# Kernel optimization log

Measured on AMD Instinct MI355X. Metric: run time of the kernel, lower is better.

## Reference

```python
import jax, jax.numpy as jnp
import numpy as np

B, N, D, TOP_K = 4, 4096, 256, 64
EPS = 1e-12  # F.normalize default eps


def setup_inputs() -> dict:
    key = jax.random.key(0)
    kx, kw, kb = jax.random.split(key, 3)
    x = jax.random.normal(kx, (B, N, D), dtype=jnp.float32)
    # value_fc: nn.Linear(in_dims, in_dims) -> weight [D, D], bias [D]
    lim = 1.0 / np.sqrt(D)
    W = jax.random.uniform(kw, (D, D), dtype=jnp.float32, minval=-lim, maxval=lim)
    b = jax.random.uniform(kb, (D,), dtype=jnp.float32, minval=-lim, maxval=lim)
    return {"x": x, "W": W, "b": b}


def reference(x, W, b):
    # value = value_fc(x)
    value = jnp.einsum("bnd,ed->bne", x, W) + b  # torch Linear: x @ W.T + b
    # F.normalize(x, p=2, dim=-1)
    norm = jnp.linalg.norm(x, axis=-1, keepdims=True)
    normed_x = x / jnp.maximum(norm, EPS)
    # full cosine-similarity matrix [B, N, N]
    cos_sim = jnp.einsum("bnd,bmd->bnm", normed_x, normed_x)
    # topk along last dim, scatter back into zeros
    topk_vals, topk_inds = jax.lax.top_k(cos_sim, TOP_K)  # [B, N, K]
    b_idx = jnp.arange(x.shape[0])[:, None, None]
    n_idx = jnp.arange(x.shape[1])[None, :, None]
    attn_sparse = jnp.zeros_like(cos_sim).at[b_idx, n_idx, topk_inds].set(topk_vals)
    # softmax over full row (zeros at non-topk positions contribute exp(0))
    attn = jax.nn.softmax(attn_sparse, axis=-1)
    return jnp.einsum("bnm,bmd->bnd", attn, value)
```

## Files before the change

### kernel.cpp

```cpp
#include <hip/hip_runtime.h>
#include <hip/hip_bf16.h>
#include <stdint.h>

#define B_ 4
#define N_ 4096
#define D_ 256
#define K_ 64
#define BN_ (B_*N_)

typedef __attribute__((ext_vector_type(8))) short bf16x8;
typedef __attribute__((ext_vector_type(8))) unsigned short u16x8;
typedef __attribute__((ext_vector_type(4))) float f32x4;
typedef __attribute__((address_space(1))) const unsigned int gas_u32;
typedef __attribute__((address_space(3))) unsigned int las_u32;

static __device__ __forceinline__ unsigned short f2bf(float f) {
  union { float f; unsigned u; } x; x.f = f;
  unsigned r = x.u + 0x7fffu + ((x.u >> 16) & 1u);
  return (unsigned short)(r >> 16);
}
static __device__ __forceinline__ float bf2f(unsigned short u) {
  union { unsigned u; float f; } x; x.u = ((unsigned)u) << 16;
  return x.f;
}
static __device__ __forceinline__ f32x4 mfma16(bf16x8 a, bf16x8 b, f32x4 c) {
  return __builtin_amdgcn_mfma_f32_16x16x32_bf16(a, b, c, 0, 0, 0);
}

__global__ __launch_bounds__(256) void prep_kernel(
    const float* __restrict__ x, const float* __restrict__ W,
    unsigned short* __restrict__ xn, float* __restrict__ norms,
    unsigned short* __restrict__ Wb, float* __restrict__ vsum) {
  const int bid = blockIdx.x;
  if (bid < 4096) {
    int row = bid * 4 + (threadIdx.x >> 6);
    int lane = threadIdx.x & 63;
    const float4 v = reinterpret_cast<const float4*>(x + (size_t)row * D_)[lane];
    float ss = v.x*v.x + v.y*v.y + v.z*v.z + v.w*v.w;
    #pragma unroll
    for (int off = 32; off > 0; off >>= 1) ss += __shfl_xor(ss, off);
    float nrm = sqrtf(ss);
    float scale = 1.0f / fmaxf(nrm, 1e-12f);
    ushort4 o;
    o.x = f2bf(v.x * scale); o.y = f2bf(v.y * scale);
    o.z = f2bf(v.z * scale); o.w = f2bf(v.w * scale);
    reinterpret_cast<ushort4*>(xn + (size_t)row * D_)[lane] = o;
    if (lane == 0) norms[row] = nrm;
  } else if (bid < 4160) {
    int i = (bid - 4096) * 256 + threadIdx.x;
    float4 v = reinterpret_cast<const float4*>(W)[i];
    ushort4 o; o.x = f2bf(v.x); o.y = f2bf(v.y); o.z = f2bf(v.z); o.w = f2bf(v.w);
    reinterpret_cast<ushort4*>(Wb)[i] = o;
  } else {
    reinterpret_cast<float4*>(vsum)[threadIdx.x] = (float4){0.f, 0.f, 0.f, 0.f};
  }
}

__global__ __launch_bounds__(256, 3) void compute_kernel(
    const unsigned short* __restrict__ xn, const float* __restrict__ norms,
    const unsigned short* __restrict__ Wb, const float* __restrict__ bias,
    unsigned short* __restrict__ value, float* __restrict__ vsum,
    unsigned short* __restrict__ S) {
  __shared__ __attribute__((aligned(16))) unsigned char smem[33792];
  unsigned char* As = smem;
  unsigned char* Bs = smem + 16384;
  float* ns_s   = (float*)(smem + 32768);
  float* bias_s = (float*)(smem + 33280);

  const int t = threadIdx.x, lane = t & 63, w = t >> 6;
  const int l15 = lane & 15, qv = lane >> 4, rb = qv * 4;
  const int wr = w >> 1, wc = w & 1;
  const int x7 = l15 & 7;

  const unsigned short* Asrc;
  const unsigned short* Bsrc;
  int rbG, cb, batch = 0;
  const bool vmode = (blockIdx.x < 256);
  if (vmode) {
    rbG = (blockIdx.x >> 1) * 128;
    cb  = (blockIdx.x & 1) * 128;
    Asrc = xn + (size_t)rbG * D_;
    Bsrc = Wb + (size_t)cb * D_;
    if (t < 128) { ns_s[t] = norms[rbG + t]; bias_s[t] = bias[cb + t]; }
  } else {
    int g = blockIdx.x - 256;
    batch = g >> 10;
    int tl = g & 1023;
    rbG = (tl >> 5) * 128;
    cb  = (tl & 31) * 128;
    Asrc = xn + ((size_t)batch * N_ + rbG) * D_;
    Bsrc = xn + ((size_t)batch * N_ + cb)  * D_;
  }

  f32x4 acc[4][4];
  #pragma unroll
  for (int i = 0; i < 4; i++)
    #pragma unroll
    for (int j = 0; j < 4; j++) acc[i][j] = (f32x4){0.f,0.f,0.f,0.f};

  for (int kk = 0; kk < 4; kk++) {
    #pragma unroll
    for (int p = 0; p < 4; p++) {
      int q = t + p * 256;
      int row = q >> 3, c = q & 7;
      int cg = (c ^ (row & 7)) * 8;
      __builtin_amdgcn_global_load_lds(
          (gas_u32*)(Asrc + (size_t)row * D_ + kk * 64 + cg),
          (las_u32*)(As + q * 16), 16, 0, 0);
      __builtin_amdgcn_global_load_lds(
          (gas_u32*)(Bsrc + (size_t)row * D_ + kk * 64 + cg),
          (las_u32*)(Bs + q * 16), 16, 0, 0);
    }
    __syncthreads();
    #pragma unroll
    for (int ks = 0; ks < 2; ks++) {
      const int cpos = (((ks * 4 + qv) ^ x7) << 4);
      bf16x8 a[4], bb[4];
      #pragma unroll
      for (int rt = 0; rt < 4; rt++)
        a[rt] = *(const bf16x8*)(As + (wr*64 + rt*16 + l15) * 128 + cpos);
      #pragma unroll
      for (int ct = 0; ct < 4; ct++)
        bb[ct] = *(const bf16x8*)(Bs + (wc*64 + ct*16 + l15) * 128 + cpos);
      #pragma unroll
      for (int rt = 0; rt < 4; rt++)
        #pragma unroll
        for (int ct = 0; ct < 4; ct++)
          acc[rt][ct] = mfma16(a[rt], bb[ct], acc[rt][ct]);
    }
    __syncthreads();
  }

  unsigned short* kbuf = (unsigned short*)smem;
  if (vmode) {
    float vpart[4] = {0.f, 0.f, 0.f, 0.f};
    #pragma unroll
    for (int rt = 0; rt < 4; rt++)
      #pragma unroll
      for (int ct = 0; ct < 4; ct++) {
        int col_l = wc*64 + ct*16 + l15;
        #pragma unroll
        for (int reg = 0; reg < 4; reg++) {
          int row_l = wr*64 + rt*16 + rb + reg;
          float v = acc[rt][ct][reg] * ns_s[row_l] + bias_s[col_l];
          int pos = (col_l & 7) | ((((col_l >> 3) ^ (row_l & 7))) << 3);
          kbuf[row_l * 128 + pos] = f2bf(v);
          vpart[ct] += v;
        }
      }
    int b2 = rbG >> 12;
    #pragma unroll
    for (int ct = 0; ct < 4; ct++)
      atomicAdd(&vsum[b2*D_ + cb + wc*64 + ct*16 + l15], vpart[ct]);
    __syncthreads();
    #pragma unroll
    for (int p = 0; p < 8; p++) {
      int q = t + p * 256;
      int row = q >> 4, c8 = q & 15;
      u16x8 d = *(const u16x8*)(kbuf + row * 128 + ((c8 ^ (row & 7)) << 3));
      *(u16x8*)(value + (size_t)(rbG + row) * D_ + cb + c8 * 8) = d;
    }
  } else {
    #pragma unroll
    for (int rt = 0; rt < 4; rt++)
      #pragma unroll
      for (int ct = 0; ct < 4; ct++) {
        int col_l = wc*64 + ct*16 + l15;
        #pragma unroll
        for (int reg = 0; reg < 4; reg++) {
          int row_l = wr*64 + rt*16 + rb + reg;
          unsigned short bits = f2bf(acc[rt][ct][reg]);
          unsigned short key = (bits & 0x8000u) ? (unsigned short)(~bits)
                                                : (unsigned short)(bits | 0x8000u);
          int pos = (col_l & 7) | ((((col_l >> 3) ^ (row_l & 7))) << 3);
          kbuf[row_l * 128 + pos] = key;
        }
      }
    __syncthreads();
    unsigned short* Sb = S + ((size_t)batch << 24);
    #pragma unroll
    for (int p = 0; p < 8; p++) {
      int q = t + p * 256;
      int row = q >> 4, c8 = q & 15;
      u16x8 d = *(const u16x8*)(kbuf + row * 128 + ((c8 ^ (row & 7)) << 3));
      *(u16x8*)(Sb + (size_t)(rbG + row) * N_ + cb + c8 * 8) = d;
    }
  }
}

__global__ __launch_bounds__(256, 8) void select_kernel(
    const unsigned short* __restrict__ S,
    const unsigned short* __restrict__ value,
    const float* __restrict__ vsum,
    float* __restrict__ out) {
  __shared__ __attribute__((aligned(16))) unsigned bb2[2][2048];
  __shared__ unsigned wt4[4];
  __shared__ float zred[4];
  __shared__ int hb_s, cg_s, lb_s, cglo_s, nsel_s, neq_s;
  __shared__ int widx_s[64];
  __shared__ float wv_s[64];
  float* partial = (float*)bb2;

  const int t = threadIdx.x, lane = t & 63, w = t >> 6;
  const int cp = w >> 1;
  const int b = blockIdx.x >> 12;
  const int r = blockIdx.x & 4095;
  const unsigned short* srow = S + ((size_t)b << 24) + ((size_t)r << 12);

  u16x8 va = *(const u16x8*)(srow + t*16);
  u16x8 vb2 = *(const u16x8*)(srow + t*16 + 8);
  unsigned ov[16];
  #pragma unroll
  for (int j = 0; j < 8; j++) { ov[j] = (unsigned short)va[j]; ov[j+8] = (unsigned short)vb2[j]; }

  #pragma unroll
  for (int p = 0; p < 4; p++)
    *(uint4*)&bb2[0][(t + p*256)*4] = (uint4){0u,0u,0u,0u};
  if (t == 0) { nsel_s = 0; neq_s = 0; }
  __syncthreads();
  #pragma unroll
  for (int j = 0; j < 16; j++) atomicAdd(&bb2[cp][ov[j] >> 5], 1u);
  __syncthreads();
  unsigned cnt[8];
  {
    uint4 c0 = *(const uint4*)&bb2[0][t*8];
    uint4 c1 = *(const uint4*)&bb2[0][t*8 + 4];
    uint4 d0 = *(const uint4*)&bb2[1][t*8];
    uint4 d1 = *(const uint4*)&bb2[1][t*8 + 4];
    cnt[0]=c0.x+d0.x; cnt[1]=c0.y+d0.y; cnt[2]=c0.z+d0.z; cnt[3]=c0.w+d0.w;
    cnt[4]=c1.x+d1.x; cnt[5]=c1.y+d1.y; cnt[6]=c1.z+d1.z; cnt[7]=c1.w+d1.w;
  }
  unsigned own = cnt[0]+cnt[1]+cnt[2]+cnt[3]+cnt[4]+cnt[5]+cnt[6]+cnt[7];
  unsigned v = own;
  #pragma unroll
  for (int off = 1; off < 64; off <<= 1) {
    unsigned o = __shfl_down(v, off);
    if (lane + off < 64) v += o;
  }
  if (lane == 0) wt4[w] = v;
  __syncthreads();
  unsigned sfx = v;
  #pragma unroll
  for (int ww = 0; ww < 4; ww++) if (ww > w) sfx += wt4[ww];
  unsigned nxt = sfx - own;
  if (sfx >= 64u && nxt < 64u) {
    unsigned c = nxt;
    #pragma unroll
    for (int jj = 7; jj >= 0; jj--) {
      unsigned cn = c + cnt[jj];
      if (cn >= 64u && c < 64u) { hb_s = t*8 + jj; cg_s = (int)c; }
      c = cn;
    }
  }
  if (t < 64) bb2[t >> 5][t & 31] = 0;
  __syncthreads();
  const unsigned hb = (unsigned)hb_s;
  const unsigned need2 = (unsigned)(64 - cg_s);
  #pragma unroll
  for (int j = 0; j < 16; j++)
    if ((ov[j] >> 5) == hb) atomicAdd(&bb2[cp][ov[j] & 31u], 1u);
  __syncthreads();
  if (w == 0) {
    unsigned own2 = 0;
    if (lane < 32) own2 = bb2[0][lane] + bb2[1][lane];
    unsigned v2 = own2;
    #pragma unroll
    for (int off = 1; off < 64; off <<= 1) {
      unsigned o = __shfl_down(v2, off);
      if (lane + off < 64) v2 += o;
    }
    unsigned nxt2 = v2 - own2;
    if (lane < 32 && v2 >= need2 && nxt2 < need2) { lb_s = lane; cglo_s = (int)nxt2; }
  }
  __syncthreads();
  const unsigned tau = (hb << 5) | (unsigned)lb_s;
  const int needeq = (int)need2 - cglo_s;

  float zloc = 0.f;
  #pragma unroll
  for (int j = 0; j < 16; j++) {
    unsigned u = ov[j];
    bool take = (u > tau);
    if (!take && u == tau) { int k = atomicAdd(&neq_s, 1); take = (k < needeq); }
    if (take) {
      int slot = atomicAdd(&nsel_s, 1);
      unsigned short bits = (u & 0x8000u) ? (unsigned short)(u & 0x7FFFu)
                                          : (unsigned short)(~u);
      float s = bf2f(bits);
      float e = __expf(s);
      zloc += e;
      widx_s[slot] = t*16 + j;
      wv_s[slot] = e - 1.0f;
    }
  }
  #pragma unroll
  for (int off = 32; off > 0; off >>= 1) zloc += __shfl_xor(zloc, off);
  if (lane == 0) zred[w] = zloc;
  __syncthreads();
  const float Z = zred[0] + zred[1] + zred[2] + zred[3] + (float)(N_ - K_);

  const size_t vbase = (size_t)b << 20;
  float ax = 0.f, ay = 0.f, az = 0.f, aw = 0.f;
  #pragma unroll
  for (int i = 0; i < 16; i++) {
    int sel = w*16 + i;
    int idx = widx_s[sel];
    float wt = wv_s[sel];
    ushort4 vv = *reinterpret_cast<const ushort4*>(&value[vbase + (size_t)idx*D_ + lane*4]);
    ax += wt * bf2f(vv.x);
    ay += wt * bf2f(vv.y);
    az += wt * bf2f(vv.z);
    aw += wt * bf2f(vv.w);
  }
  partial[w*256 + lane*4 + 0] = ax;
  partial[w*256 + lane*4 + 1] = ay;
  partial[w*256 + lane*4 + 2] = az;
  partial[w*256 + lane*4 + 3] = aw;
  __syncthreads();
  float ps = partial[t] + partial[256 + t] + partial[512 + t] + partial[768 + t];
  out[(((size_t)b << 12) + r) * D_ + t] = (ps + vsum[b*D_ + t]) * (1.0f / Z);
}

extern "C" void kernel_launch(void* const* d_in, const int* in_sizes, int n_in,
                              void* d_out, int out_size, void* d_ws, size_t ws_size,
                              hipStream_t stream) {
  const float* x    = (const float*)d_in[0];
  const float* W    = (const float*)d_in[1];
  const float* bias = (const float*)d_in[2];
  float* out = (float*)d_out;
  char* ws = (char*)d_ws;
  unsigned short* xn    = (unsigned short*)(ws);
  unsigned short* Wb    = (unsigned short*)(ws + 8388608);
  float*          norms = (float*)(ws + 8519680);
  unsigned short* value = (unsigned short*)(ws + 8585216);
  float*          vsum  = (float*)(ws + 16973824);
  unsigned short* S     = (unsigned short*)(ws + 16977920);

  prep_kernel<<<4161, 256, 0, stream>>>(x, W, xn, norms, Wb, vsum);
  compute_kernel<<<4352, 256, 0, stream>>>(xn, norms, Wb, bias, value, vsum, S);
  select_kernel<<<BN_, 256, 0, stream>>>(S, value, vsum, out);
}
```

Baseline: 222.0 us.

## Process one row per wavefront in top-k select and prefetch next K-stage in GEMM

The select kernel now assigns one row per 64-lane wavefront, four rows per block, instead of one row per 256-thread block. It uses per-wave packed 16-bit histograms and shuffle-based scans, which removes most block-wide barriers and shared-memory round trips. The compute kernel loads the current stage's LDS fragments into registers first, then issues the global-to-LDS loads for the next K stage before running the MFMAs, so the copy overlaps the math. The cost is higher register pressure from holding 32 key values plus the fragment arrays, and more LDS atomics per wave.

```diff
diff --git a/kernel.cpp b/kernel.cpp
--- a/kernel.cpp
+++ b/kernel.cpp
@@ -92,13 +92,7 @@
     Bsrc = xn + ((size_t)batch * N_ + cb)  * D_;
   }
 
-  f32x4 acc[4][4];
-  #pragma unroll
-  for (int i = 0; i < 4; i++)
-    #pragma unroll
-    for (int j = 0; j < 4; j++) acc[i][j] = (f32x4){0.f,0.f,0.f,0.f};
-
-  for (int kk = 0; kk < 4; kk++) {
+  auto STAGE = [&](int kk) {
     #pragma unroll
     for (int p = 0; p < 4; p++) {
       int q = t + p * 256;
@@ -111,24 +105,38 @@
           (gas_u32*)(Bsrc + (size_t)row * D_ + kk * 64 + cg),
           (las_u32*)(Bs + q * 16), 16, 0, 0);
     }
-    __syncthreads();
+  };
+
+  f32x4 acc[4][4];
+  #pragma unroll
+  for (int i = 0; i < 4; i++)
+    #pragma unroll
+    for (int j = 0; j < 4; j++) acc[i][j] = (f32x4){0.f,0.f,0.f,0.f};
+
+  STAGE(0);
+  __syncthreads();
+  for (int kk = 0; kk < 4; kk++) {
+    bf16x8 afr[2][4], bfr[2][4];
     #pragma unroll
     for (int ks = 0; ks < 2; ks++) {
       const int cpos = (((ks * 4 + qv) ^ x7) << 4);
-      bf16x8 a[4], bb[4];
       #pragma unroll
       for (int rt = 0; rt < 4; rt++)
-        a[rt] = *(const bf16x8*)(As + (wr*64 + rt*16 + l15) * 128 + cpos);
+        afr[ks][rt] = *(const bf16x8*)(As + (wr*64 + rt*16 + l15) * 128 + cpos);
       #pragma unroll
       for (int ct = 0; ct < 4; ct++)
-        bb[ct] = *(const bf16x8*)(Bs + (wc*64 + ct*16 + l15) * 128 + cpos);
+        bfr[ks][ct] = *(const bf16x8*)(Bs + (wc*64 + ct*16 + l15) * 128 + cpos);
+    }
+    __syncthreads();
+    if (kk < 3) STAGE(kk + 1);
+    #pragma unroll
+    for (int ks = 0; ks < 2; ks++)
       #pragma unroll
       for (int rt = 0; rt < 4; rt++)
         #pragma unroll
         for (int ct = 0; ct < 4; ct++)
-          acc[rt][ct] = mfma16(a[rt], bb[ct], acc[rt][ct]);
-    }
-    __syncthreads();
+          acc[rt][ct] = mfma16(afr[ks][rt], bfr[ks][ct], acc[rt][ct]);
+    if (kk < 3) __syncthreads();
   }
 
   unsigned short* kbuf = (unsigned short*)smem;
@@ -188,137 +196,145 @@
   }
 }
 
-__global__ __launch_bounds__(256, 8) void select_kernel(
+__global__ __launch_bounds__(256) void select_kernel(
     const unsigned short* __restrict__ S,
     const unsigned short* __restrict__ value,
     const float* __restrict__ vsum,
     float* __restrict__ out) {
-  __shared__ __attribute__((aligned(16))) unsigned bb2[2][2048];
-  __shared__ unsigned wt4[4];
-  __shared__ float zred[4];
-  __shared__ int hb_s, cg_s, lb_s, cglo_s, nsel_s, neq_s;
-  __shared__ int widx_s[64];
-  __shared__ float wv_s[64];
-  float* partial = (float*)bb2;
+  __shared__ unsigned hist[4][1024];
+  __shared__ unsigned pair2[4][64][2];
+  __shared__ int cnts[4][2];
 
   const int t = threadIdx.x, lane = t & 63, w = t >> 6;
-  const int cp = w >> 1;
-  const int b = blockIdx.x >> 12;
-  const int r = blockIdx.x & 4095;
+  const int rowg = blockIdx.x * 4 + w;
+  const int b = rowg >> 12;
+  const int r = rowg & 4095;
   const unsigned short* srow = S + ((size_t)b << 24) + ((size_t)r << 12);
 
-  u16x8 va = *(const u16x8*)(srow + t*16);
-  u16x8 vb2 = *(const u16x8*)(srow + t*16 + 8);
-  unsigned ov[16];
-  #pragma unroll
-  for (int j = 0; j < 8; j++) { ov[j] = (unsigned short)va[j]; ov[j+8] = (unsigned short)vb2[j]; }
+  uint4 kq[8];
+  #pragma unroll
+  for (int c = 0; c < 8; c++)
+    kq[c] = *(const uint4*)(srow + c*512 + lane*8);
 
   #pragma unroll
   for (int p = 0; p < 4; p++)
-    *(uint4*)&bb2[0][(t + p*256)*4] = (uint4){0u,0u,0u,0u};
-  if (t == 0) { nsel_s = 0; neq_s = 0; }
-  __syncthreads();
-  #pragma unroll
-  for (int j = 0; j < 16; j++) atomicAdd(&bb2[cp][ov[j] >> 5], 1u);
-  __syncthreads();
-  unsigned cnt[8];
-  {
-    uint4 c0 = *(const uint4*)&bb2[0][t*8];
-    uint4 c1 = *(const uint4*)&bb2[0][t*8 + 4];
-    uint4 d0 = *(const uint4*)&bb2[1][t*8];
-    uint4 d1 = *(const uint4*)&bb2[1][t*8 + 4];
-    cnt[0]=c0.x+d0.x; cnt[1]=c0.y+d0.y; cnt[2]=c0.z+d0.z; cnt[3]=c0.w+d0.w;
-    cnt[4]=c1.x+d1.x; cnt[5]=c1.y+d1.y; cnt[6]=c1.z+d1.z; cnt[7]=c1.w+d1.w;
-  }
-  unsigned own = cnt[0]+cnt[1]+cnt[2]+cnt[3]+cnt[4]+cnt[5]+cnt[6]+cnt[7];
-  unsigned v = own;
+    *(uint4*)&hist[w][lane*16 + p*4] = (uint4){0u,0u,0u,0u};
+  if (lane == 0) { cnts[w][0] = 0; cnts[w][1] = 0; }
+
+  #pragma unroll
+  for (int c = 0; c < 8; c++) {
+    unsigned uu[4] = {kq[c].x, kq[c].y, kq[c].z, kq[c].w};
+    #pragma unroll
+    for (int m = 0; m < 4; m++) {
+      unsigned u = uu[m];
+      atomicAdd(&hist[w][(u & 0xffffu) >> 6], 1u << (((u >> 5) & 1u) * 16));
+      atomicAdd(&hist[w][u >> 22],            1u << (((u >> 21) & 1u) * 16));
+    }
+  }
+
+  unsigned hw[16];
+  #pragma unroll
+  for (int p = 0; p < 4; p++)
+    *(uint4*)&hw[p*4] = *(const uint4*)&hist[w][lane*16 + p*4];
+  unsigned ltot = 0;
+  #pragma unroll
+  for (int i = 0; i < 16; i++) ltot += (hw[i] & 0xffffu) + (hw[i] >> 16);
+
+  unsigned v = ltot;
   #pragma unroll
   for (int off = 1; off < 64; off <<= 1) {
     unsigned o = __shfl_down(v, off);
     if (lane + off < 64) v += o;
   }
-  if (lane == 0) wt4[w] = v;
-  __syncthreads();
-  unsigned sfx = v;
-  #pragma unroll
-  for (int ww = 0; ww < 4; ww++) if (ww > w) sfx += wt4[ww];
-  unsigned nxt = sfx - own;
-  if (sfx >= 64u && nxt < 64u) {
-    unsigned c = nxt;
-    #pragma unroll
-    for (int jj = 7; jj >= 0; jj--) {
-      unsigned cn = c + cnt[jj];
-      if (cn >= 64u && c < 64u) { hb_s = t*8 + jj; cg_s = (int)c; }
+  unsigned above = v - ltot;
+  int pk = -1;
+  if (v >= 64u && above < 64u) {
+    unsigned c = above; int hbl = 0; unsigned cgl = 0;
+    #pragma unroll
+    for (int j = 31; j >= 0; j--) {
+      unsigned cj = (j & 1) ? (hw[j >> 1] >> 16) : (hw[j >> 1] & 0xffffu);
+      unsigned cn = c + cj;
+      if (cn >= 64u && c < 64u) { hbl = lane*32 + j; cgl = c; }
       c = cn;
     }
-  }
-  if (t < 64) bb2[t >> 5][t & 31] = 0;
-  __syncthreads();
-  const unsigned hb = (unsigned)hb_s;
-  const unsigned need2 = (unsigned)(64 - cg_s);
-  #pragma unroll
-  for (int j = 0; j < 16; j++)
-    if ((ov[j] >> 5) == hb) atomicAdd(&bb2[cp][ov[j] & 31u], 1u);
-  __syncthreads();
-  if (w == 0) {
-    unsigned own2 = 0;
-    if (lane < 32) own2 = bb2[0][lane] + bb2[1][lane];
-    unsigned v2 = own2;
-    #pragma unroll
-    for (int off = 1; off < 64; off <<= 1) {
-      unsigned o = __shfl_down(v2, off);
-      if (lane + off < 64) v2 += o;
-    }
-    unsigned nxt2 = v2 - own2;
-    if (lane < 32 && v2 >= need2 && nxt2 < need2) { lb_s = lane; cglo_s = (int)nxt2; }
-  }
-  __syncthreads();
-  const unsigned tau = (hb << 5) | (unsigned)lb_s;
-  const int needeq = (int)need2 - cglo_s;
+    pk = (hbl << 6) | (int)cgl;
+  }
+  #pragma unroll
+  for (int off = 1; off < 64; off <<= 1) pk = max(pk, __shfl_xor(pk, off));
+  const unsigned hb = (unsigned)(pk >> 6);
+  const unsigned need2 = 64u - (unsigned)(pk & 63);
+
+  if (lane < 16) hist[w][lane] = 0;
+  #pragma unroll
+  for (int c = 0; c < 8; c++) {
+    unsigned uu[4] = {kq[c].x, kq[c].y, kq[c].z, kq[c].w};
+    #pragma unroll
+    for (int m = 0; m < 4; m++) {
+      unsigned klo = uu[m] & 0xffffu, khi = uu[m] >> 16;
+      if ((klo >> 5) == hb) atomicAdd(&hist[w][(klo & 31u) >> 1], 1u << ((klo & 1u) * 16));
+      if ((khi >> 5) == hb) atomicAdd(&hist[w][(khi & 31u) >> 1], 1u << ((khi & 1u) * 16));
+    }
+  }
+  unsigned wv2 = hist[w][lane >> 1];
+  unsigned c2 = (lane & 1) ? (wv2 >> 16) : (wv2 & 0xffffu);
+  unsigned s2 = c2;
+  #pragma unroll
+  for (int off = 1; off < 32; off <<= 1) {
+    unsigned o = __shfl_down(s2, off);
+    if (lane + off < 32) s2 += o;
+  }
+  unsigned ab2 = s2 - c2;
+  int pk2 = -1;
+  if (lane < 32 && s2 >= need2 && ab2 < need2) pk2 = (lane << 6) | (int)ab2;
+  #pragma unroll
+  for (int off = 1; off < 64; off <<= 1) pk2 = max(pk2, __shfl_xor(pk2, off));
+  const unsigned tau = (hb << 5) | (unsigned)(pk2 >> 6);
+  const int needeq = (int)need2 - (pk2 & 63);
 
   float zloc = 0.f;
   #pragma unroll
-  for (int j = 0; j < 16; j++) {
-    unsigned u = ov[j];
-    bool take = (u > tau);
-    if (!take && u == tau) { int k = atomicAdd(&neq_s, 1); take = (k < needeq); }
-    if (take) {
-      int slot = atomicAdd(&nsel_s, 1);
-      unsigned short bits = (u & 0x8000u) ? (unsigned short)(u & 0x7FFFu)
-                                          : (unsigned short)(~u);
-      float s = bf2f(bits);
-      float e = __expf(s);
-      zloc += e;
-      widx_s[slot] = t*16 + j;
-      wv_s[slot] = e - 1.0f;
+  for (int c = 0; c < 8; c++) {
+    int cb0 = c*512 + lane*8;
+    unsigned uu[4] = {kq[c].x, kq[c].y, kq[c].z, kq[c].w};
+    #pragma unroll
+    for (int m = 0; m < 4; m++) {
+      #pragma unroll
+      for (int h = 0; h < 2; h++) {
+        unsigned key = h ? (uu[m] >> 16) : (uu[m] & 0xffffu);
+        bool take = key > tau;
+        if (!take && key == tau) { int k = atomicAdd(&cnts[w][1], 1); take = (k < needeq); }
+        if (take) {
+          int slot = atomicAdd(&cnts[w][0], 1);
+          unsigned short bits = (key & 0x8000u) ? (unsigned short)(key & 0x7fffu)
+                                                : (unsigned short)(~key);
+          float e = __expf(bf2f(bits));
+          zloc += e;
+          pair2[w][slot][0] = (unsigned)(cb0 + m*2 + h) << 9;
+          pair2[w][slot][1] = __float_as_uint(e - 1.0f);
+        }
+      }
     }
   }
   #pragma unroll
   for (int off = 32; off > 0; off >>= 1) zloc += __shfl_xor(zloc, off);
-  if (lane == 0) zred[w] = zloc;
-  __syncthreads();
-  const float Z = zred[0] + zred[1] + zred[2] + zred[3] + (float)(N_ - K_);
-
-  const size_t vbase = (size_t)b << 20;
-  float ax = 0.f, ay = 0.f, az = 0.f, aw = 0.f;
-  #pragma unroll
-  for (int i = 0; i < 16; i++) {
-    int sel = w*16 + i;
-    int idx = widx_s[sel];
-    float wt = wv_s[sel];
-    ushort4 vv = *reinterpret_cast<const ushort4*>(&value[vbase + (size_t)idx*D_ + lane*4]);
-    ax += wt * bf2f(vv.x);
-    ay += wt * bf2f(vv.y);
-    az += wt * bf2f(vv.z);
-    aw += wt * bf2f(vv.w);
-  }
-  partial[w*256 + lane*4 + 0] = ax;
-  partial[w*256 + lane*4 + 1] = ay;
-  partial[w*256 + lane*4 + 2] = az;
-  partial[w*256 + lane*4 + 3] = aw;
-  __syncthreads();
-  float ps = partial[t] + partial[256 + t] + partial[512 + t] + partial[768 + t];
-  out[(((size_t)b << 12) + r) * D_ + t] = (ps + vsum[b*D_ + t]) * (1.0f / Z);
+  const float invZ = 1.0f / (zloc + (float)(N_ - K_));
+
+  const char* vbb = (const char*)value + ((size_t)b << 21);
+  float a0 = 0.f, a1 = 0.f, a2 = 0.f, a3 = 0.f;
+  for (int i = 0; i < 64; i++) {
+    uint2 pr = *(const uint2*)&pair2[w][i][0];
+    float wt = __uint_as_float(pr.y);
+    uint2 vv = *(const uint2*)(vbb + pr.x + lane*8);
+    a0 += wt * __uint_as_float(vv.x << 16);
+    a1 += wt * __uint_as_float(vv.x & 0xffff0000u);
+    a2 += wt * __uint_as_float(vv.y << 16);
+    a3 += wt * __uint_as_float(vv.y & 0xffff0000u);
+  }
+  float4 vs = *(const float4*)(vsum + b*D_ + lane*4);
+  float4 o;
+  o.x = (a0 + vs.x) * invZ; o.y = (a1 + vs.y) * invZ;
+  o.z = (a2 + vs.z) * invZ; o.w = (a3 + vs.w) * invZ;
+  *(float4*)(out + (size_t)rowg * D_ + lane*4) = o;
 }
 
 extern "C" void kernel_launch(void* const* d_in, const int* in_sizes, int n_in,
@@ -338,5 +354,5 @@
 
   prep_kernel<<<4161, 256, 0, stream>>>(x, W, xn, norms, Wb, vsum);
   compute_kernel<<<4352, 256, 0, stream>>>(xn, norms, Wb, bias, value, vsum, S);
-  select_kernel<<<BN_, 256, 0, stream>>>(S, value, vsum, out);
-}
+  select_kernel<<<BN_/4, 256, 0, stream>>>(S, value, vsum, out);
+}
```

New measurement: 211.7 us. -4.6%, faster.
